# Performance work log

Measured on AMD Instinct MI355X. Metric: run time of the kernel, lower is better.

## Reference

```python
import jax, jax.numpy as jnp
import numpy as np

BINS = 10


def setup_inputs() -> dict:
    key = jax.random.key(0)
    k1, k2 = jax.random.split(key)
    x = jax.random.uniform(k1, (16384, 2048), dtype=jnp.float32, minval=1e-4, maxval=1.0 - 1e-4)
    target = jax.random.uniform(k2, (16384, 2048), dtype=jnp.float32)
    return {"x": x, "target": target}


def reference(x, target):
    # gradient magnitude (detached in original)
    g = jnp.abs(jax.lax.stop_gradient(x) - target)
    # _g2bin: floor(g * (bins - 0.0001)) -> integer bin ids in [0, BINS-1]
    bin_idx = jnp.floor(g * (BINS - 1e-4)).astype(jnp.int32)
    # histogram (replaces the serialized per-bin python loop)
    bin_count = jnp.bincount(bin_idx.ravel(), length=BINS).astype(jnp.float32)
    N = x.shape[0] * x.shape[1]
    nonempty_bins = jnp.sum(bin_count > 0).astype(jnp.float32)
    gd = jnp.clip(bin_count * nonempty_bins, 1.0, None)
    beta = N / gd  # [BINS]
    # BCE on probabilities, reweighted by gathered beta
    loss = -(target * jnp.log(x) + (1.0 - target) * jnp.log(1.0 - x))
    loss = loss * beta[bin_idx]
    return jnp.mean(loss)
```

## Files before the change

### kernel.cpp

```cpp
#include <hip/hip_runtime.h>

#define BINS 10

__device__ __forceinline__ void accum_elem(float xx, float tt,
                                           float* __restrict__ sum,
                                           unsigned* __restrict__ cnt) {
    float g = fabsf(xx - tt);
    int b = (int)(g * 9.9999f);
    b = b > (BINS - 1) ? (BINS - 1) : b;
    float loss = -(tt * __logf(xx) + (1.0f - tt) * __logf(1.0f - xx));
#pragma unroll
    for (int k = 0; k < BINS; ++k) {
        bool m = (b == k);
        sum[k] += m ? loss : 0.0f;
        cnt[k] += m ? 1u : 0u;
    }
}

__global__ __launch_bounds__(256) void ghm_partial(
    const float* __restrict__ x, const float* __restrict__ t,
    float* __restrict__ psum, unsigned* __restrict__ pcnt,
    int n4, long long n_total)
{
    float sum[BINS];
    unsigned cnt[BINS];
#pragma unroll
    for (int k = 0; k < BINS; ++k) { sum[k] = 0.0f; cnt[k] = 0u; }

    const float4* __restrict__ x4 = (const float4*)x;
    const float4* __restrict__ t4 = (const float4*)t;
    int tid = blockIdx.x * blockDim.x + threadIdx.x;
    int stride = gridDim.x * blockDim.x;

    for (int i = tid; i < n4; i += stride) {
        float4 xv = x4[i];
        float4 tv = t4[i];
        accum_elem(xv.x, tv.x, sum, cnt);
        accum_elem(xv.y, tv.y, sum, cnt);
        accum_elem(xv.z, tv.z, sum, cnt);
        accum_elem(xv.w, tv.w, sum, cnt);
    }
    long long tail_base = (long long)n4 * 4;
    long long rem = n_total - tail_base;
    if ((long long)tid < rem) {
        accum_elem(x[tail_base + tid], t[tail_base + tid], sum, cnt);
    }

#pragma unroll
    for (int k = 0; k < BINS; ++k) {
#pragma unroll
        for (int off = 32; off > 0; off >>= 1) {
            sum[k] += __shfl_down(sum[k], off, 64);
            cnt[k] += (unsigned)__shfl_down((int)cnt[k], off, 64);
        }
    }

    __shared__ float s_sum[4][BINS];
    __shared__ unsigned s_cnt[4][BINS];
    int lane = threadIdx.x & 63;
    int wv = threadIdx.x >> 6;
    if (lane == 0) {
#pragma unroll
        for (int k = 0; k < BINS; ++k) { s_sum[wv][k] = sum[k]; s_cnt[wv][k] = cnt[k]; }
    }
    __syncthreads();
    if (threadIdx.x < BINS) {
        float s = 0.0f;
        unsigned c = 0u;
#pragma unroll
        for (int w = 0; w < 4; ++w) { s += s_sum[w][threadIdx.x]; c += s_cnt[w][threadIdx.x]; }
        psum[(size_t)blockIdx.x * BINS + threadIdx.x] = s;
        pcnt[(size_t)blockIdx.x * BINS + threadIdx.x] = c;
    }
}

__global__ __launch_bounds__(256) void ghm_final(
    const float* __restrict__ psum, const unsigned* __restrict__ pcnt,
    float* __restrict__ out, int nblocks, float Nf)
{
    float sum[BINS];
    unsigned cnt[BINS];
#pragma unroll
    for (int k = 0; k < BINS; ++k) { sum[k] = 0.0f; cnt[k] = 0u; }

    for (int i = threadIdx.x; i < nblocks; i += blockDim.x) {
#pragma unroll
        for (int k = 0; k < BINS; ++k) {
            sum[k] += psum[(size_t)i * BINS + k];
            cnt[k] += pcnt[(size_t)i * BINS + k];
        }
    }

#pragma unroll
    for (int k = 0; k < BINS; ++k) {
#pragma unroll
        for (int off = 32; off > 0; off >>= 1) {
            sum[k] += __shfl_down(sum[k], off, 64);
            cnt[k] += (unsigned)__shfl_down((int)cnt[k], off, 64);
        }
    }

    __shared__ float s_sum[4][BINS];
    __shared__ unsigned s_cnt[4][BINS];
    int lane = threadIdx.x & 63;
    int wv = threadIdx.x >> 6;
    if (lane == 0) {
#pragma unroll
        for (int k = 0; k < BINS; ++k) { s_sum[wv][k] = sum[k]; s_cnt[wv][k] = cnt[k]; }
    }
    __syncthreads();

    if (threadIdx.x == 0) {
        float tot_s[BINS];
        unsigned tot_c[BINS];
#pragma unroll
        for (int k = 0; k < BINS; ++k) {
            float s = 0.0f;
            unsigned c = 0u;
#pragma unroll
            for (int w = 0; w < 4; ++w) { s += s_sum[w][k]; c += s_cnt[w][k]; }
            tot_s[k] = s;
            tot_c[k] = c;
        }
        float nonempty = 0.0f;
#pragma unroll
        for (int k = 0; k < BINS; ++k) nonempty += (tot_c[k] > 0u) ? 1.0f : 0.0f;
        float total = 0.0f;
#pragma unroll
        for (int k = 0; k < BINS; ++k) {
            float gd = (float)tot_c[k] * nonempty;
            gd = gd < 1.0f ? 1.0f : gd;
            float beta = Nf / gd;
            total += tot_s[k] * beta;
        }
        out[0] = total / Nf;
    }
}

extern "C" void kernel_launch(void* const* d_in, const int* in_sizes, int n_in,
                              void* d_out, int out_size, void* d_ws, size_t ws_size,
                              hipStream_t stream) {
    const float* x = (const float*)d_in[0];
    const float* t = (const float*)d_in[1];
    float* out = (float*)d_out;

    long long N = (long long)in_sizes[0];
    int n4 = (int)(N / 4);

    int nblocks = 2048;
    size_t per_block = (size_t)BINS * (sizeof(float) + sizeof(unsigned));
    size_t maxb = ws_size / per_block;
    if ((size_t)nblocks > maxb) nblocks = (int)maxb;
    if (nblocks < 1) nblocks = 1;

    float* psum = (float*)d_ws;
    unsigned* pcnt = (unsigned*)(psum + (size_t)nblocks * BINS);

    ghm_partial<<<nblocks, 256, 0, stream>>>(x, t, psum, pcnt, n4, N);
    ghm_final<<<1, 256, 0, stream>>>(psum, pcnt, out, nblocks, (float)N);
}
```

Before: 285.2 us.

## Replace per-thread register bin masks with replicated LDS atomic histograms

Per-element binning no longer does ten masked register adds per element. Each element now does a float and an integer atomicAdd into a per-lane shared-memory histogram row, with 64 replicas padded to stride 11 so lanes land in different banks. The loss is rewritten as a single FMA with the sign applied once at the end, and the partials are stored bin-major for the final kernel. The cost is two LDS atomics per element, which will likely be slower than the register selects in this memory-bound kernel. Lanes from the four wavefronts of a block also share the same row, so atomics contend across waves.

```diff
diff --git a/kernel.cpp b/kernel.cpp
--- a/kernel.cpp
+++ b/kernel.cpp
@@ -1,31 +1,37 @@
 #include <hip/hip_runtime.h>
 
 #define BINS 10
+#define REPL 64
+#define RSTRIDE 11
+#define NWORDS (REPL * RSTRIDE)
 
 __device__ __forceinline__ void accum_elem(float xx, float tt,
-                                           float* __restrict__ sum,
-                                           unsigned* __restrict__ cnt) {
+                                           float* __restrict__ myrow,
+                                           unsigned* __restrict__ myrowc) {
     float g = fabsf(xx - tt);
     int b = (int)(g * 9.9999f);
-    b = b > (BINS - 1) ? (BINS - 1) : b;
-    float loss = -(tt * __logf(xx) + (1.0f - tt) * __logf(1.0f - xx));
-#pragma unroll
-    for (int k = 0; k < BINS; ++k) {
-        bool m = (b == k);
-        sum[k] += m ? loss : 0.0f;
-        cnt[k] += m ? 1u : 0u;
-    }
+    float om = 1.0f - xx;
+    float l1 = __logf(xx);
+    float l2 = __logf(om);
+    float s = __builtin_fmaf(tt, l1 - l2, l2);
+    atomicAdd(&myrow[b], s);
+    atomicAdd(&myrowc[b], 1u);
 }
 
 __global__ __launch_bounds__(256) void ghm_partial(
     const float* __restrict__ x, const float* __restrict__ t,
     float* __restrict__ psum, unsigned* __restrict__ pcnt,
-    int n4, long long n_total)
+    int n4, long long n_total, int nblocks)
 {
-    float sum[BINS];
-    unsigned cnt[BINS];
-#pragma unroll
-    for (int k = 0; k < BINS; ++k) { sum[k] = 0.0f; cnt[k] = 0u; }
+    __shared__ float ls[NWORDS];
+    __shared__ unsigned lc[NWORDS];
+
+    for (int i = threadIdx.x; i < NWORDS; i += 256) { ls[i] = 0.0f; lc[i] = 0u; }
+    __syncthreads();
+
+    const int lane = threadIdx.x & 63;
+    float* __restrict__ myrow = &ls[lane * RSTRIDE];
+    unsigned* __restrict__ myrowc = &lc[lane * RSTRIDE];
 
     const float4* __restrict__ x4 = (const float4*)x;
     const float4* __restrict__ t4 = (const float4*)t;
@@ -35,23 +41,69 @@
     for (int i = tid; i < n4; i += stride) {
         float4 xv = x4[i];
         float4 tv = t4[i];
-        accum_elem(xv.x, tv.x, sum, cnt);
-        accum_elem(xv.y, tv.y, sum, cnt);
-        accum_elem(xv.z, tv.z, sum, cnt);
-        accum_elem(xv.w, tv.w, sum, cnt);
+        accum_elem(xv.x, tv.x, myrow, myrowc);
+        accum_elem(xv.y, tv.y, myrow, myrowc);
+        accum_elem(xv.z, tv.z, myrow, myrowc);
+        accum_elem(xv.w, tv.w, myrow, myrowc);
     }
     long long tail_base = (long long)n4 * 4;
     long long rem = n_total - tail_base;
     if ((long long)tid < rem) {
-        accum_elem(x[tail_base + tid], t[tail_base + tid], sum, cnt);
+        accum_elem(x[tail_base + tid], t[tail_base + tid], myrow, myrowc);
+    }
+
+    __syncthreads();
+
+    if (threadIdx.x < 64) {
+        float s[BINS];
+        unsigned c[BINS];
+#pragma unroll
+        for (int b = 0; b < BINS; ++b) {
+            s[b] = ls[lane * RSTRIDE + b];
+            c[b] = lc[lane * RSTRIDE + b];
+        }
+#pragma unroll
+        for (int b = 0; b < BINS; ++b) {
+#pragma unroll
+            for (int off = 32; off > 0; off >>= 1) {
+                s[b] += __shfl_down(s[b], off, 64);
+                c[b] += (unsigned)__shfl_down((int)c[b], off, 64);
+            }
+        }
+        if (lane == 0) {
+#pragma unroll
+            for (int b = 0; b < BINS; ++b) {
+                psum[(size_t)b * nblocks + blockIdx.x] = s[b];
+                pcnt[(size_t)b * nblocks + blockIdx.x] = c[b];
+            }
+        }
+    }
+}
+
+__global__ __launch_bounds__(256) void ghm_final(
+    const float* __restrict__ psum, const unsigned* __restrict__ pcnt,
+    float* __restrict__ out, int nblocks, float Nf)
+{
+    float bs[BINS];
+    unsigned bc[BINS];
+#pragma unroll
+    for (int b = 0; b < BINS; ++b) {
+        float s = 0.0f;
+        unsigned c = 0u;
+        for (int i = threadIdx.x; i < nblocks; i += 256) {
+            s += psum[(size_t)b * nblocks + i];
+            c += pcnt[(size_t)b * nblocks + i];
+        }
+        bs[b] = s;
+        bc[b] = c;
     }
 
 #pragma unroll
-    for (int k = 0; k < BINS; ++k) {
+    for (int b = 0; b < BINS; ++b) {
 #pragma unroll
         for (int off = 32; off > 0; off >>= 1) {
-            sum[k] += __shfl_down(sum[k], off, 64);
-            cnt[k] += (unsigned)__shfl_down((int)cnt[k], off, 64);
+            bs[b] += __shfl_down(bs[b], off, 64);
+            bc[b] += (unsigned)__shfl_down((int)bc[b], off, 64);
         }
     }
 
@@ -61,79 +113,32 @@
     int wv = threadIdx.x >> 6;
     if (lane == 0) {
 #pragma unroll
-        for (int k = 0; k < BINS; ++k) { s_sum[wv][k] = sum[k]; s_cnt[wv][k] = cnt[k]; }
-    }
-    __syncthreads();
-    if (threadIdx.x < BINS) {
-        float s = 0.0f;
-        unsigned c = 0u;
-#pragma unroll
-        for (int w = 0; w < 4; ++w) { s += s_sum[w][threadIdx.x]; c += s_cnt[w][threadIdx.x]; }
-        psum[(size_t)blockIdx.x * BINS + threadIdx.x] = s;
-        pcnt[(size_t)blockIdx.x * BINS + threadIdx.x] = c;
-    }
-}
-
-__global__ __launch_bounds__(256) void ghm_final(
-    const float* __restrict__ psum, const unsigned* __restrict__ pcnt,
-    float* __restrict__ out, int nblocks, float Nf)
-{
-    float sum[BINS];
-    unsigned cnt[BINS];
-#pragma unroll
-    for (int k = 0; k < BINS; ++k) { sum[k] = 0.0f; cnt[k] = 0u; }
-
-    for (int i = threadIdx.x; i < nblocks; i += blockDim.x) {
-#pragma unroll
-        for (int k = 0; k < BINS; ++k) {
-            sum[k] += psum[(size_t)i * BINS + k];
-            cnt[k] += pcnt[(size_t)i * BINS + k];
-        }
-    }
-
-#pragma unroll
-    for (int k = 0; k < BINS; ++k) {
-#pragma unroll
-        for (int off = 32; off > 0; off >>= 1) {
-            sum[k] += __shfl_down(sum[k], off, 64);
-            cnt[k] += (unsigned)__shfl_down((int)cnt[k], off, 64);
-        }
-    }
-
-    __shared__ float s_sum[4][BINS];
-    __shared__ unsigned s_cnt[4][BINS];
-    int lane = threadIdx.x & 63;
-    int wv = threadIdx.x >> 6;
-    if (lane == 0) {
-#pragma unroll
-        for (int k = 0; k < BINS; ++k) { s_sum[wv][k] = sum[k]; s_cnt[wv][k] = cnt[k]; }
+        for (int b = 0; b < BINS; ++b) { s_sum[wv][b] = bs[b]; s_cnt[wv][b] = bc[b]; }
     }
     __syncthreads();
 
     if (threadIdx.x == 0) {
+        float nonempty = 0.0f;
         float tot_s[BINS];
         unsigned tot_c[BINS];
 #pragma unroll
-        for (int k = 0; k < BINS; ++k) {
+        for (int b = 0; b < BINS; ++b) {
             float s = 0.0f;
             unsigned c = 0u;
 #pragma unroll
-            for (int w = 0; w < 4; ++w) { s += s_sum[w][k]; c += s_cnt[w][k]; }
-            tot_s[k] = s;
-            tot_c[k] = c;
+            for (int w = 0; w < 4; ++w) { s += s_sum[w][b]; c += s_cnt[w][b]; }
+            tot_s[b] = s;
+            tot_c[b] = c;
+            nonempty += (c > 0u) ? 1.0f : 0.0f;
         }
-        float nonempty = 0.0f;
-#pragma unroll
-        for (int k = 0; k < BINS; ++k) nonempty += (tot_c[k] > 0u) ? 1.0f : 0.0f;
         float total = 0.0f;
 #pragma unroll
-        for (int k = 0; k < BINS; ++k) {
-            float gd = (float)tot_c[k] * nonempty;
+        for (int b = 0; b < BINS; ++b) {
+            float gd = (float)tot_c[b] * nonempty;
             gd = gd < 1.0f ? 1.0f : gd;
-            float beta = Nf / gd;
-            total += tot_s[k] * beta;
+            total += tot_s[b] * (Nf / gd);
         }
-        out[0] = total / Nf;
+        out[0] = -total / Nf;
     }
 }
 
@@ -154,8 +159,8 @@
     if (nblocks < 1) nblocks = 1;
 
     float* psum = (float*)d_ws;
-    unsigned* pcnt = (unsigned*)(psum + (size_t)nblocks * BINS);
+    unsigned* pcnt = (unsigned*)(psum + (size_t)BINS * nblocks);
 
-    ghm_partial<<<nblocks, 256, 0, stream>>>(x, t, psum, pcnt, n4, N);
+    ghm_partial<<<nblocks, 256, 0, stream>>>(x, t, psum, pcnt, n4, N, nblocks);
     ghm_final<<<1, 256, 0, stream>>>(psum, pcnt, out, nblocks, (float)N);
 }
```

After: 379.9 us. 33.2% more time.
